# Optimization experiments

Hardware: AMD Instinct MI355X
Metric: run time of the kernel (lower is better)

Reference implementation:

```python
import jax, jax.numpy as jnp
import numpy as np

N1, N2, D = 8192, 8192, 128

def setup_inputs() -> dict:
    key = jax.random.key(0)
    k1, k2 = jax.random.split(key)
    desc1 = jax.random.normal(k1, (N1, D), dtype=jnp.float32)
    desc2 = jax.random.normal(k2, (N2, D), dtype=jnp.float32)
    return {"desc1": desc1, "desc2": desc2}

def reference(desc1, desc2):
    # sim: [N1, N2] descriptor similarity matrix
    sim = desc1 @ desc2.T
    # mutual nearest-neighbor matching ('nnm' mode)
    nn12 = jnp.argmax(sim, axis=1)            # [N1] best match in image 2 for each kp in image 1
    nn21 = jnp.argmax(sim, axis=0)            # [N2] best match in image 1 for each kp in image 2
    ids1 = jnp.arange(sim.shape[0])
    mutual = nn21[nn12] == ids1               # mutual-consistency check
    # dense jit-friendly encoding of the ragged match list: -1 where no mutual match
    matches0 = jnp.where(mutual, nn12, -1)    # [N1] int
    # matching_scores0 = top-1 similarity per row (torch.topk(..., k=1)[0].squeeze())
    scores = jnp.max(sim, axis=1)             # [N1]
    return matches0, scores
```

## Files before the change

kernel.cpp:

```cpp
#include <hip/hip_runtime.h>
#include <stdint.h>

#define N1 8192
#define N2 8192
#define DK 128
#define TAU 0.08f
#define BIAS 256.0f
#define LDR 132

typedef _Float16 half8 __attribute__((ext_vector_type(8)));
typedef _Float16 half4 __attribute__((ext_vector_type(4)));
typedef float floatx4 __attribute__((ext_vector_type(4)));

__device__ __align__(16) _Float16 g_Af[N1 * DK];
__device__ __align__(16) _Float16 g_Bf[N2 * DK];
__device__ __align__(16) float2 g_rowtop2[64 * N1];
__device__ __align__(16) float2 g_coltop2[64 * N2];
__device__ int g_nn12[N1];
__device__ int g_nn21[N2];

__device__ __forceinline__ float bkey(float v, unsigned idx) {
    unsigned b = __float_as_uint(v + BIAS);
    return __uint_as_float((b & 0xFFFFFF80u) | idx);
}
__device__ __forceinline__ float bval(float key) {
    return __uint_as_float(__float_as_uint(key) & 0xFFFFFF80u);
}
__device__ __forceinline__ int bidx(float key) {
    return (int)(__float_as_uint(key) & 127u);
}
__device__ __forceinline__ void push2f(float& t1, float& t2, float p) {
    float m = __builtin_amdgcn_fmed3f(t1, t2, p);
    t1 = fmaxf(t1, p);
    t2 = m;
}
__device__ __forceinline__ void merge2f(float& t1, float& t2, float o1, float o2) {
    float x = fmaxf(t2, o2);
    float m = __builtin_amdgcn_fmed3f(t1, o1, x);
    t1 = fmaxf(t1, o1);
    t2 = m;
}
__device__ __forceinline__ unsigned mono32(float v) {
    unsigned u = __float_as_uint(v);
    return u ^ ((u & 0x80000000u) ? 0xFFFFFFFFu : 0x80000000u);
}
__device__ __forceinline__ float unmono32(unsigned k) {
    unsigned u = (k & 0x80000000u) ? (k ^ 0x80000000u) : ~k;
    return __uint_as_float(u);
}
__device__ __forceinline__ unsigned long long pack64(float d, unsigned idx) {
    return ((unsigned long long)mono32(d) << 32) | (unsigned)(~idx);
}

__global__ __launch_bounds__(256) void convert_kernel(const float* __restrict__ A,
                                                      const float* __restrict__ B) {
    int t = blockIdx.x * blockDim.x + threadIdx.x;
    const int perMat = N1 * (DK / 4);
    int which = (t >= perMat) ? 1 : 0;
    const float* src = which ? B : A;
    _Float16* dst = which ? g_Bf : g_Af;
    int i = which ? t - perMat : t;
    int m = i >> 5;
    int kq = i & 31;
    float4 v = *reinterpret_cast<const float4*>(src + (size_t)m * DK + kq * 4);
    half4 h = {(_Float16)v.x, (_Float16)v.y, (_Float16)v.z, (_Float16)v.w};
    *reinterpret_cast<half4*>(dst + (size_t)m * DK + kq * 4) = h;
}

__global__ __launch_bounds__(256) void simf16_kernel() {
    __shared__ _Float16 Bs[128 * LDR];
    __shared__ float2 lmerge[2][128];

    const int tid  = threadIdx.x;
    const int lane = tid & 63;
    const int wave = tid >> 6;
    const int wm = wave >> 1, wn = wave & 1;
    const int fr = lane & 15, q = lane >> 4;

    const int flat = blockIdx.y * 64 + blockIdx.x;
    const int xcd = flat & 7;
    const int j = flat >> 3;
    const int ty = j >> 3;
    const int tx = ((j & 7) << 3) | xcd;
    const int row0 = ty * 128, col0 = tx * 128;

#pragma unroll
    for (int i = 0; i < 8; ++i) {
        int f = i * 256 + tid;
        int r = f >> 4, c = f & 15;
        *reinterpret_cast<float4*>(&Bs[r * LDR + c * 8]) =
            *reinterpret_cast<const float4*>(g_Bf + (size_t)(col0 + r) * DK + c * 8);
    }

    floatx4 acc[4][4];
#pragma unroll
    for (int mt = 0; mt < 4; ++mt)
#pragma unroll
        for (int nt = 0; nt < 4; ++nt)
            acc[mt][nt] = (floatx4){0.f, 0.f, 0.f, 0.f};

    const _Float16* Abase = g_Af + (size_t)(row0 + wm * 64 + fr) * DK + q * 8;

    half8 af[4], afn[4];
#pragma unroll
    for (int mt = 0; mt < 4; ++mt)
        af[mt] = *reinterpret_cast<const half8*>(Abase + mt * 16 * DK);

    __syncthreads();

#pragma unroll
    for (int ks = 0; ks < 4; ++ks) {
        if (ks < 3) {
#pragma unroll
            for (int mt = 0; mt < 4; ++mt)
                afn[mt] = *reinterpret_cast<const half8*>(Abase + mt * 16 * DK + (ks + 1) * 32);
        }
        half8 bf[4];
#pragma unroll
        for (int nt = 0; nt < 4; ++nt)
            bf[nt] = *reinterpret_cast<const half8*>(&Bs[(wn * 64 + nt * 16 + fr) * LDR + ks * 32 + q * 8]);
#pragma unroll
        for (int mt = 0; mt < 4; ++mt)
#pragma unroll
            for (int nt = 0; nt < 4; ++nt)
                acc[mt][nt] = __builtin_amdgcn_mfma_f32_16x16x32_f16(af[mt], bf[nt], acc[mt][nt], 0, 0, 0);
        if (ks < 3) {
#pragma unroll
            for (int mt = 0; mt < 4; ++mt)
                af[mt] = afn[mt];
        }
    }

#pragma unroll
    for (int mt = 0; mt < 4; ++mt) {
#pragma unroll
        for (int reg = 0; reg < 4; ++reg) {
            float t1 = 0.f, t2 = 0.f;
#pragma unroll
            for (int nt = 0; nt < 4; ++nt)
                push2f(t1, t2, bkey(acc[mt][nt][reg], (unsigned)(wn * 64 + nt * 16 + fr)));
#pragma unroll
            for (int off = 1; off < 16; off <<= 1) {
                float o1 = __shfl_xor(t1, off, 64);
                float o2 = __shfl_xor(t2, off, 64);
                merge2f(t1, t2, o1, o2);
            }
            if (fr == 0) lmerge[wn][wm * 64 + mt * 16 + q * 4 + reg] = make_float2(t1, t2);
        }
    }
    __syncthreads();
    if (tid < 128) {
        float2 a = lmerge[0][tid], b = lmerge[1][tid];
        merge2f(a.x, a.y, b.x, b.y);
        g_rowtop2[(size_t)tx * N1 + row0 + tid] = a;
    }
    __syncthreads();

#pragma unroll
    for (int nt = 0; nt < 4; ++nt) {
        float t1 = 0.f, t2 = 0.f;
#pragma unroll
        for (int mt = 0; mt < 4; ++mt)
#pragma unroll
            for (int reg = 0; reg < 4; ++reg)
                push2f(t1, t2, bkey(acc[mt][nt][reg], (unsigned)(wm * 64 + mt * 16 + q * 4 + reg)));
        float o1 = __shfl_xor(t1, 16, 64), o2 = __shfl_xor(t2, 16, 64);
        merge2f(t1, t2, o1, o2);
        o1 = __shfl_xor(t1, 32, 64); o2 = __shfl_xor(t2, 32, 64);
        merge2f(t1, t2, o1, o2);
        if (q == 0) lmerge[wm][wn * 64 + nt * 16 + fr] = make_float2(t1, t2);
    }
    __syncthreads();
    if (tid < 128) {
        float2 a = lmerge[0][tid], b = lmerge[1][tid];
        merge2f(a.x, a.y, b.x, b.y);
        g_coltop2[(size_t)ty * N2 + col0 + tid] = a;
    }
}

__global__ __launch_bounds__(256) void fix_kernel(const float* __restrict__ A,
                                                  const float* __restrict__ B,
                                                  float* __restrict__ out) {
    __shared__ float2 tile[64 * 16];
    __shared__ unsigned long long slot[16];
    __shared__ int cand[256];
    __shared__ int cand_cnt;

    const int tid = threadIdx.x;
    const bool rowside = blockIdx.x >= 512;
    const int base0 = (blockIdx.x & 511) * 16;
    const float2* top2 = rowside ? g_rowtop2 : g_coltop2;

#pragma unroll
    for (int i = 0; i < 4; ++i) {
        int idx = i * 256 + tid;
        int grp = idx >> 4, c = idx & 15;
        tile[grp * 16 + c] = top2[(size_t)grp * N1 + base0 + c];
    }
    if (tid < 16) slot[tid] = 0ULL;
    if (tid == 0) cand_cnt = 0;
    __syncthreads();

    const int c = tid >> 4, j = tid & 15;
    float mx = 0.f;
#pragma unroll
    for (int s = 0; s < 4; ++s)
        mx = fmaxf(mx, tile[(j * 4 + s) * 16 + c].x);
    mx = fmaxf(mx, __shfl_xor(mx, 1, 64));
    mx = fmaxf(mx, __shfl_xor(mx, 2, 64));
    mx = fmaxf(mx, __shfl_xor(mx, 4, 64));
    mx = fmaxf(mx, __shfl_xor(mx, 8, 64));
    const float thr = bval(mx) - TAU;
#pragma unroll
    for (int s = 0; s < 4; ++s) {
        int grp = j * 4 + s;
        float2 e = tile[grp * 16 + c];
        if (bval(e.x) >= thr) {
            int o = grp * 128 + bidx(e.x);
            int si = atomicAdd(&cand_cnt, 1);
            if (si < 256) cand[si] = (c << 16) | o;
        }
        if (bval(e.y) >= thr) {
            int o = grp * 128 + bidx(e.y);
            int si = atomicAdd(&cand_cnt, 1);
            if (si < 256) cand[si] = (c << 16) | o;
        }
    }
    __syncthreads();

    const int nc = min(cand_cnt, 256);
    for (int i = tid; i < nc; i += 256) {
        int pc = cand[i];
        int cl = pc >> 16, other = pc & 0xFFFF;
        const float* ar = rowside ? (A + (size_t)(base0 + cl) * DK) : (A + (size_t)other * DK);
        const float* br = rowside ? (B + (size_t)other * DK) : (B + (size_t)(base0 + cl) * DK);
        float d = 0.0f;
#pragma unroll
        for (int k4 = 0; k4 < DK / 4; ++k4) {
            float4 a = *reinterpret_cast<const float4*>(ar + k4 * 4);
            float4 b = *reinterpret_cast<const float4*>(br + k4 * 4);
            d = fmaf(a.x, b.x, d);
            d = fmaf(a.y, b.y, d);
            d = fmaf(a.z, b.z, d);
            d = fmaf(a.w, b.w, d);
        }
        atomicMax(&slot[cl], pack64(d, (unsigned)other));
    }
    __syncthreads();

    if (tid < 16) {
        unsigned long long p = slot[tid];
        int idx = base0 + tid;
        if (rowside) {
            g_nn12[idx] = (int)(~(unsigned)p);
            out[N1 + idx] = unmono32((unsigned)(p >> 32));
        } else {
            g_nn21[idx] = (int)(~(unsigned)p);
        }
    }
}

__global__ __launch_bounds__(256) void mutual_kernel(float* __restrict__ out) {
    int i = blockIdx.x * blockDim.x + threadIdx.x;
    if (i < N1) {
        int m = g_nn12[i];
        out[i] = (float)((g_nn21[m] == i) ? m : -1);
    }
}

extern "C" void kernel_launch(void* const* d_in, const int* in_sizes, int n_in,
                              void* d_out, int out_size, void* d_ws, size_t ws_size,
                              hipStream_t stream) {
    const float* A = (const float*)d_in[0];
    const float* B = (const float*)d_in[1];
    float* out = (float*)d_out;

    convert_kernel<<<2 * N1 * (DK / 4) / 256, 256, 0, stream>>>(A, B);
    dim3 grid(64, 64);
    simf16_kernel<<<grid, 256, 0, stream>>>();
    fix_kernel<<<1024, 256, 0, stream>>>(A, B, out);
    mutual_kernel<<<N1 / 256, 256, 0, stream>>>(out);
}
```

Measured before the change: 127.3 us.

## Halve B shared tile, load in two passes, raise occupancy hint

The B tile in shared memory shrinks from 128 to 64 rows and is loaded in two passes, each covering half of every wave's column range, with a barrier between passes. The A fragments are re-streamed from global memory in the second pass. Launch bounds now request 5 blocks per CU, which the smaller LDS footprint allows. This trades extra barriers, a second pass of A loads and possible register pressure for higher occupancy to hide latency.

```diff
diff --git a/kernel.cpp b/kernel.cpp
--- a/kernel.cpp
+++ b/kernel.cpp
@@ -67,8 +67,8 @@
     *reinterpret_cast<half4*>(dst + (size_t)m * DK + kq * 4) = h;
 }
 
-__global__ __launch_bounds__(256) void simf16_kernel() {
-    __shared__ _Float16 Bs[128 * LDR];
+__global__ __launch_bounds__(256, 5) void simf16_kernel() {
+    __shared__ _Float16 Bs[64 * LDR];
     __shared__ float2 lmerge[2][128];
 
     const int tid  = threadIdx.x;
@@ -84,14 +84,6 @@
     const int tx = ((j & 7) << 3) | xcd;
     const int row0 = ty * 128, col0 = tx * 128;
 
-#pragma unroll
-    for (int i = 0; i < 8; ++i) {
-        int f = i * 256 + tid;
-        int r = f >> 4, c = f & 15;
-        *reinterpret_cast<float4*>(&Bs[r * LDR + c * 8]) =
-            *reinterpret_cast<const float4*>(g_Bf + (size_t)(col0 + r) * DK + c * 8);
-    }
-
     floatx4 acc[4][4];
 #pragma unroll
     for (int mt = 0; mt < 4; ++mt)
@@ -102,32 +94,49 @@
     const _Float16* Abase = g_Af + (size_t)(row0 + wm * 64 + fr) * DK + q * 8;
 
     half8 af[4], afn[4];
-#pragma unroll
-    for (int mt = 0; mt < 4; ++mt)
-        af[mt] = *reinterpret_cast<const half8*>(Abase + mt * 16 * DK);
-
-    __syncthreads();
-
-#pragma unroll
-    for (int ks = 0; ks < 4; ++ks) {
-        if (ks < 3) {
+
+#pragma unroll
+    for (int p = 0; p < 2; ++p) {
+        if (p) __syncthreads();
+
+#pragma unroll
+        for (int i = 0; i < 4; ++i) {
+            int f = i * 256 + tid;
+            int r = f >> 4, c = f & 15;
+            int g = ((r >> 5) << 6) + p * 32 + (r & 31);
+            *reinterpret_cast<float4*>(&Bs[r * LDR + c * 8]) =
+                *reinterpret_cast<const float4*>(g_Bf + (size_t)(col0 + g) * DK + c * 8);
+        }
+
+        if (p == 0) {
 #pragma unroll
             for (int mt = 0; mt < 4; ++mt)
-                afn[mt] = *reinterpret_cast<const half8*>(Abase + mt * 16 * DK + (ks + 1) * 32);
-        }
-        half8 bf[4];
-#pragma unroll
-        for (int nt = 0; nt < 4; ++nt)
-            bf[nt] = *reinterpret_cast<const half8*>(&Bs[(wn * 64 + nt * 16 + fr) * LDR + ks * 32 + q * 8]);
-#pragma unroll
-        for (int mt = 0; mt < 4; ++mt)
-#pragma unroll
-            for (int nt = 0; nt < 4; ++nt)
-                acc[mt][nt] = __builtin_amdgcn_mfma_f32_16x16x32_f16(af[mt], bf[nt], acc[mt][nt], 0, 0, 0);
-        if (ks < 3) {
-#pragma unroll
-            for (int mt = 0; mt < 4; ++mt)
-                af[mt] = afn[mt];
+                af[mt] = *reinterpret_cast<const half8*>(Abase + mt * 16 * DK);
+        }
+
+        __syncthreads();
+
+#pragma unroll
+        for (int ks = 0; ks < 4; ++ks) {
+            const bool pref = (ks < 3) || (p == 0);
+            if (pref) {
+                int nko = ((ks + 1) & 3) * 32;
+#pragma unroll
+                for (int mt = 0; mt < 4; ++mt)
+                    afn[mt] = *reinterpret_cast<const half8*>(Abase + mt * 16 * DK + nko);
+            }
+            half8 bf0 = *reinterpret_cast<const half8*>(&Bs[(wn * 32 + fr) * LDR + ks * 32 + q * 8]);
+            half8 bf1 = *reinterpret_cast<const half8*>(&Bs[(wn * 32 + 16 + fr) * LDR + ks * 32 + q * 8]);
+#pragma unroll
+            for (int mt = 0; mt < 4; ++mt) {
+                acc[mt][2 * p]     = __builtin_amdgcn_mfma_f32_16x16x32_f16(af[mt], bf0, acc[mt][2 * p], 0, 0, 0);
+                acc[mt][2 * p + 1] = __builtin_amdgcn_mfma_f32_16x16x32_f16(af[mt], bf1, acc[mt][2 * p + 1], 0, 0, 0);
+            }
+            if (pref) {
+#pragma unroll
+                for (int mt = 0; mt < 4; ++mt)
+                    af[mt] = afn[mt];
+            }
         }
     }
 
```

Result: slower. 162.7 us (+27.7%).
